# Kernel optimization log

Measured on AMD Instinct MI355X. Metric: run time of the kernel, lower is better.

The kernel has to match this reference:

```python
import jax, jax.numpy as jnp
import numpy as np

N = 50000
IN_C = 128
HID = 64
HEADS = 4
OUT_C = 64
E_RAND = 800000
NEG_SLOPE = 0.2  # PyG GATConv default


def setup_inputs() -> dict:
    key = jax.random.key(0)
    ks = jax.random.split(key, 10)
    x = jax.random.normal(ks[0], (N, IN_C), dtype=jnp.float32)
    src = jax.random.randint(ks[1], (E_RAND,), 0, N)
    dst = jax.random.randint(ks[2], (E_RAND,), 0, N)
    loops = jnp.arange(N)
    # PyG GATConv adds self-loops by default; append them here
    edge_index = jnp.stack([jnp.concatenate([src, loops]),
                            jnp.concatenate([dst, loops])], axis=0).astype(jnp.int64)
    s = 0.05
    W1 = jax.random.normal(ks[3], (IN_C, HEADS * HID), dtype=jnp.float32) * s
    att_src1 = jax.random.normal(ks[4], (HEADS, HID), dtype=jnp.float32) * s
    att_dst1 = jax.random.normal(ks[5], (HEADS, HID), dtype=jnp.float32) * s
    b1 = jnp.zeros((HEADS * HID,), dtype=jnp.float32)
    W2 = jax.random.normal(ks[6], (HEADS * HID, OUT_C), dtype=jnp.float32) * s
    att_src2 = jax.random.normal(ks[7], (1, OUT_C), dtype=jnp.float32) * s
    att_dst2 = jax.random.normal(ks[8], (1, OUT_C), dtype=jnp.float32) * s
    b2 = jnp.zeros((OUT_C,), dtype=jnp.float32)
    return {"x": x, "edge_index": edge_index, "W1": W1, "att_src1": att_src1,
            "att_dst1": att_dst1, "b1": b1, "W2": W2, "att_src2": att_src2,
            "att_dst2": att_dst2, "b2": b2}


def gat_conv(x, src, dst, W, att_src, att_dst, bias, heads, ch, concat):
    n = x.shape[0]
    h = (x @ W).reshape(n, heads, ch)                      # [N,H,C]
    a_src = jnp.einsum('nhc,hc->nh', h, att_src)           # [N,H]
    a_dst = jnp.einsum('nhc,hc->nh', h, att_dst)
    e = jax.nn.leaky_relu(a_src[src] + a_dst[dst], NEG_SLOPE)  # [E,H]
    # segment softmax over incoming edges of each dst node
    m = jax.ops.segment_max(e, dst, num_segments=n)
    ex = jnp.exp(e - m[dst])
    ssum = jax.ops.segment_sum(ex, dst, num_segments=n)
    alpha = ex / jnp.where(ssum[dst] > 0, ssum[dst], 1.0)  # [E,H]
    msg = h[src] * alpha[:, :, None]                        # [E,H,C]
    out = jax.ops.segment_sum(msg, dst, num_segments=n)     # [N,H,C]
    out = out.reshape(n, heads * ch) if concat else out.mean(axis=1)
    return out + bias


def reference(x, edge_index, W1, att_src1, att_dst1, b1, W2, att_src2, att_dst2, b2):
    src, dst = edge_index[0], edge_index[1]
    # eval mode: feature dropout and attention dropout are identity
    h = gat_conv(x, src, dst, W1, att_src1, att_dst1, b1, HEADS, HID, True)
    h = jax.nn.elu(h)
    out = gat_conv(h, src, dst, W2, att_src2, att_dst2, b2, 1, OUT_C, False)
    return out
```

## Files before the change

kernel.cpp:

```cpp
#include <hip/hip_runtime.h>
#include <hip/hip_bf16.h>

#define IN_C 128
#define HID 64
#define HEADS 4
#define OUT_C 64
#define NEG_SLOPE 0.2f

typedef __attribute__((ext_vector_type(8))) short bfrag8;
typedef __attribute__((ext_vector_type(4))) float facc4;

__device__ __forceinline__ float bf16u_to_f(unsigned short u) {
  return __uint_as_float(((unsigned)u) << 16);
}
__device__ __forceinline__ float lof(unsigned u) {
  return __uint_as_float(u << 16);
}
__device__ __forceinline__ float hif(unsigned u) {
  return __uint_as_float(u & 0xffff0000u);
}
__device__ __forceinline__ unsigned short f_to_bf16u(float f) {
  return __bfloat16_as_ushort(__float2bfloat16(f));
}
__device__ __forceinline__ float leaky(float x) {
  return (x > 0.f) ? x : NEG_SLOPE * x;
}

__global__ __launch_bounds__(256) void setup_kernel(
    const float* __restrict__ W1, const float* __restrict__ W2,
    unsigned short* __restrict__ B1img, unsigned short* __restrict__ B2img,
    int* __restrict__ deg, int n) {
  int bid = blockIdx.x;
  if (bid < 24) {
    int i = bid * 256 + threadIdx.x;
    if (i < 4096) {
      int g = i & 7, nn = (i >> 3) & 255, kt = i >> 11;
      unsigned short q[8];
#pragma unroll
      for (int e = 0; e < 8; ++e)
        q[e] = f_to_bf16u(W1[(size_t)(kt * 64 + g * 8 + e) * 256 + nn]);
      *reinterpret_cast<uint4*>(
          &B1img[kt * 16384 + nn * 64 + ((g ^ (nn & 7)) << 3)]) =
          *reinterpret_cast<const uint4*>(q);
    } else if (i < 4096 + 2048) {
      int j = i - 4096;
      int g = j & 7, nn = (j >> 3) & 63, kt = j >> 9;
      unsigned short q[8];
#pragma unroll
      for (int e = 0; e < 8; ++e)
        q[e] = f_to_bf16u(W2[(size_t)(kt * 64 + g * 8 + e) * 64 + nn]);
      *reinterpret_cast<uint4*>(
          &B2img[kt * 4096 + nn * 64 + ((g ^ (nn & 7)) << 3)]) =
          *reinterpret_cast<const uint4*>(q);
    }
  } else {
    int i = (bid - 24) * 1024 + threadIdx.x * 4;
    if (i < n)
      *reinterpret_cast<int4*>(&deg[i]) = make_int4(0, 0, 0, 0);
  }
}

__global__ __launch_bounds__(256) void gemm1_hist_kernel(
    const float* __restrict__ A, const unsigned short* __restrict__ B1img,
    const float* __restrict__ att_src, const float* __restrict__ att_dst,
    unsigned short* __restrict__ Hout, float* __restrict__ a_src,
    float* __restrict__ a_dst, int M, int G1,
    const int* __restrict__ dst, int E, int* __restrict__ deg,
    int* __restrict__ rank) {
  __shared__ unsigned short As[64 * 64];
  __shared__ unsigned short Bs[256 * 64];
  const int t = threadIdx.x;

  if ((int)blockIdx.x >= G1) {
    int e0 = ((int)blockIdx.x - G1) * 1024 + t * 4;
    if (e0 + 3 < E) {
      int4 d4 = *reinterpret_cast<const int4*>(&dst[e0]);
      int4 r4;
      r4.x = atomicAdd(&deg[d4.x], 1);
      r4.y = atomicAdd(&deg[d4.y], 1);
      r4.z = atomicAdd(&deg[d4.z], 1);
      r4.w = atomicAdd(&deg[d4.w], 1);
      *reinterpret_cast<int4*>(&rank[e0]) = r4;
    } else {
      for (int e = e0; e < E; ++e) rank[e] = atomicAdd(&deg[dst[e]], 1);
    }
    return;
  }

  const int wid = t >> 6, lane = t & 63;
  const int lg = lane >> 4, li = lane & 15;
  const int bm = blockIdx.x * 64;

  facc4 acc[16];
#pragma unroll
  for (int fn = 0; fn < 16; ++fn) acc[fn] = (facc4)(0.f);

#pragma unroll
  for (int kt = 0; kt < 2; ++kt) {
#pragma unroll
    for (int p = 0; p < 2; ++p) {
      int flat = t + p * 256;
      int row = flat >> 3, g = flat & 7;
      int gr = bm + row;
      float4 v0 = make_float4(0.f, 0.f, 0.f, 0.f), v1 = v0;
      if (gr < M) {
        const float* src = &A[(size_t)gr * 128 + kt * 64 + g * 8];
        v0 = *reinterpret_cast<const float4*>(src);
        v1 = *reinterpret_cast<const float4*>(src + 4);
      }
      unsigned short q[8];
      q[0] = f_to_bf16u(v0.x); q[1] = f_to_bf16u(v0.y);
      q[2] = f_to_bf16u(v0.z); q[3] = f_to_bf16u(v0.w);
      q[4] = f_to_bf16u(v1.x); q[5] = f_to_bf16u(v1.y);
      q[6] = f_to_bf16u(v1.z); q[7] = f_to_bf16u(v1.w);
      *reinterpret_cast<uint4*>(&As[row * 64 + ((g ^ (row & 7)) << 3)]) =
          *reinterpret_cast<const uint4*>(q);
    }
#pragma unroll
    for (int p = 0; p < 8; ++p) {
      int gi = t + p * 256;
      *reinterpret_cast<uint4*>(&Bs[gi * 8]) =
          *reinterpret_cast<const uint4*>(&B1img[kt * 16384 + gi * 8]);
    }
    __syncthreads();
#pragma unroll
    for (int ks = 0; ks < 2; ++ks) {
      int arow = wid * 16 + li;
      int gk = ks * 4 + lg;
      bfrag8 a = *reinterpret_cast<const bfrag8*>(
          &As[arow * 64 + ((gk ^ (arow & 7)) << 3)]);
#pragma unroll
      for (int fn = 0; fn < 16; ++fn) {
        int col = fn * 16 + li;
        bfrag8 b = *reinterpret_cast<const bfrag8*>(
            &Bs[col * 64 + ((gk ^ (col & 7)) << 3)]);
        acc[fn] =
            __builtin_amdgcn_mfma_f32_16x16x32_bf16(a, b, acc[fn], 0, 0, 0);
      }
    }
    __syncthreads();
  }

#pragma unroll
  for (int reg = 0; reg < 4; ++reg) {
    int row = bm + wid * 16 + lg * 4 + reg;
    if (row < M) {
#pragma unroll
      for (int fn = 0; fn < 16; ++fn)
        Hout[(size_t)row * 256 + fn * 16 + li] = f_to_bf16u(acc[fn][reg]);
    }
#pragma unroll
    for (int h = 0; h < 4; ++h) {
      float ps = 0.f, pd = 0.f;
#pragma unroll
      for (int q = 0; q < 4; ++q) {
        int fn = h * 4 + q;
        float c = acc[fn][reg];
        ps += c * att_src[fn * 16 + li];
        pd += c * att_dst[fn * 16 + li];
      }
#pragma unroll
      for (int m = 1; m < 16; m <<= 1) {
        ps += __shfl_xor(ps, m);
        pd += __shfl_xor(pd, m);
      }
      if (row < M && li == 0) {
        a_src[(size_t)row * 4 + h] = ps;
        a_dst[(size_t)row * 4 + h] = pd;
      }
    }
  }
}

__global__ __launch_bounds__(256) void mfma_gemm2(
    const unsigned short* __restrict__ A, const unsigned short* __restrict__ B2img,
    const float* __restrict__ att_src, const float* __restrict__ att_dst,
    unsigned short* __restrict__ Hout, float* __restrict__ a_src,
    float* __restrict__ a_dst, int M) {
  __shared__ unsigned short As[64 * 64];
  __shared__ unsigned short Bs[64 * 64];
  const int t = threadIdx.x;
  const int wid = t >> 6, lane = t & 63;
  const int lg = lane >> 4, li = lane & 15;
  const int bm = blockIdx.x * 64;

  facc4 acc[4];
#pragma unroll
  for (int fn = 0; fn < 4; ++fn) acc[fn] = (facc4)(0.f);

#pragma unroll
  for (int kt = 0; kt < 4; ++kt) {
#pragma unroll
    for (int p = 0; p < 2; ++p) {
      int flat = t + p * 256;
      int row = flat >> 3, g = flat & 7;
      int gr = bm + row;
      uint4 v = make_uint4(0, 0, 0, 0);
      if (gr < M)
        v = *reinterpret_cast<const uint4*>(&A[(size_t)gr * 256 + kt * 64 + g * 8]);
      *reinterpret_cast<uint4*>(&As[row * 64 + ((g ^ (row & 7)) << 3)]) = v;
    }
#pragma unroll
    for (int p = 0; p < 2; ++p) {
      int gi = t + p * 256;
      *reinterpret_cast<uint4*>(&Bs[gi * 8]) =
          *reinterpret_cast<const uint4*>(&B2img[kt * 4096 + gi * 8]);
    }
    __syncthreads();
#pragma unroll
    for (int ks = 0; ks < 2; ++ks) {
      int arow = wid * 16 + li;
      int gk = ks * 4 + lg;
      bfrag8 a = *reinterpret_cast<const bfrag8*>(
          &As[arow * 64 + ((gk ^ (arow & 7)) << 3)]);
#pragma unroll
      for (int fn = 0; fn < 4; ++fn) {
        int col = fn * 16 + li;
        bfrag8 b = *reinterpret_cast<const bfrag8*>(
            &Bs[col * 64 + ((gk ^ (col & 7)) << 3)]);
        acc[fn] =
            __builtin_amdgcn_mfma_f32_16x16x32_bf16(a, b, acc[fn], 0, 0, 0);
      }
    }
    __syncthreads();
  }

  float s_att[4], d_att[4];
#pragma unroll
  for (int fn = 0; fn < 4; ++fn) {
    s_att[fn] = att_src[fn * 16 + li];
    d_att[fn] = att_dst[fn * 16 + li];
  }
#pragma unroll
  for (int reg = 0; reg < 4; ++reg) {
    int row = bm + wid * 16 + lg * 4 + reg;
    float ps = 0.f, pd = 0.f;
#pragma unroll
    for (int fn = 0; fn < 4; ++fn) {
      float c = acc[fn][reg];
      ps += c * s_att[fn];
      pd += c * d_att[fn];
    }
#pragma unroll
    for (int m = 1; m < 16; m <<= 1) {
      ps += __shfl_xor(ps, m);
      pd += __shfl_xor(pd, m);
    }
    if (row < M) {
#pragma unroll
      for (int fn = 0; fn < 4; ++fn)
        Hout[(size_t)row * 64 + fn * 16 + li] = f_to_bf16u(acc[fn][reg]);
      if (li == 0) {
        a_src[row] = ps;
        a_dst[row] = pd;
      }
    }
  }
}

__device__ __forceinline__ int pad4(int d) { return (d + 3) & ~3; }

__global__ __launch_bounds__(256) void scan_partial_kernel(
    const int* __restrict__ deg, int n, int* __restrict__ partials) {
  __shared__ int sm[256];
  int t = threadIdx.x;
  int i = blockIdx.x * 256 + t;
  sm[t] = (i < n) ? pad4(deg[i]) : 0;
  __syncthreads();
  for (int off = 128; off > 0; off >>= 1) {
    if (t < off) sm[t] += sm[t + off];
    __syncthreads();
  }
  if (t == 0) partials[blockIdx.x] = sm[0];
}

__global__ __launch_bounds__(256) void scan_expand_kernel(
    const int* __restrict__ deg, int n, const int* __restrict__ partials,
    int nb, int* __restrict__ offsets, int* __restrict__ ssrc) {
  __shared__ int smp[256];
  __shared__ int sm[256];
  int t = threadIdx.x;
  smp[t] = (t < nb) ? partials[t] : 0;
  __syncthreads();
  for (int off = 1; off < 256; off <<= 1) {
    int u = (t >= off) ? smp[t - off] : 0;
    __syncthreads();
    smp[t] += u;
    __syncthreads();
  }
  int base = (blockIdx.x > 0) ? smp[blockIdx.x - 1] : 0;
  int i = blockIdx.x * 256 + t;
  int d = (i < n) ? deg[i] : 0;
  int v = pad4(d);
  sm[t] = v;
  __syncthreads();
  for (int off = 1; off < 256; off <<= 1) {
    int u = (t >= off) ? sm[t - off] : 0;
    __syncthreads();
    sm[t] += u;
    __syncthreads();
  }
  int excl = sm[t] - v + base;
  if (i < n) {
    offsets[i] = excl;
    for (int k = d; k < v; ++k) ssrc[excl + k] = -1;
  }
}

__global__ void scatter_kernel(const int* __restrict__ src,
                               const int* __restrict__ dst,
                               const int* __restrict__ rank,
                               const int* __restrict__ offsets, int E,
                               int* __restrict__ ssrc) {
  int e0 = (blockIdx.x * blockDim.x + threadIdx.x) * 4;
  if (e0 + 3 < E) {
    int4 s4 = *reinterpret_cast<const int4*>(&src[e0]);
    int4 d4 = *reinterpret_cast<const int4*>(&dst[e0]);
    int4 r4 = *reinterpret_cast<const int4*>(&rank[e0]);
    ssrc[offsets[d4.x] + r4.x] = s4.x;
    ssrc[offsets[d4.y] + r4.y] = s4.y;
    ssrc[offsets[d4.z] + r4.z] = s4.z;
    ssrc[offsets[d4.w] + r4.w] = s4.w;
  } else {
    for (int e = e0; e < E; ++e) ssrc[offsets[dst[e]] + rank[e]] = src[e];
  }
}

__global__ __launch_bounds__(256) void agg1_kernel(
    const unsigned short* __restrict__ h1, const float* __restrict__ as1,
    const float* __restrict__ ad1, const int* __restrict__ ssrc,
    const int* __restrict__ offsets, const int* __restrict__ deg,
    const float* __restrict__ bias, unsigned short* __restrict__ out,
    int n_nodes) {
  int wave = (int)((blockIdx.x * blockDim.x + threadIdx.x) >> 6);
  int lane = threadIdx.x & 63;
  if (wave >= n_nodes) return;
  int head = lane >> 4;
  int off = offsets[wave];
  int cnt = deg[wave];
  int last = ((cnt + 3) >> 2) - 1;
  const int* S_ = ssrc + off;
  float ad = ad1[wave * 4 + head];
  const int pbase = lane & 48;

  auto ldS = [&](int g) {
    return *reinterpret_cast<const int4*>(S_ + min(g, last) * 4);
  };
  auto gK = [&](int4 S, float* a_out) {
    int sk = (lane & 1) ? S.y : S.x;
    int sk2 = (lane & 1) ? S.w : S.z;
    sk = (lane & 2) ? sk2 : sk;
    *a_out = as1[max(sk, 0) * 4 + head];
    return sk;
  };
  auto mkP = [&](int sk, float a) {
    float pk = (sk >= 0) ? __expf(leaky(a + ad)) : 0.f;
    return make_float4(__shfl(pk, pbase), __shfl(pk, pbase + 1),
                       __shfl(pk, pbase + 2), __shfl(pk, pbase + 3));
  };
  auto gat = [&](int s) {
    return *reinterpret_cast<const uint2*>(
        &h1[(size_t)max(s, 0) * 256 + lane * 4]);
  };

  float l = 0.f, a0 = 0.f, a1 = 0.f, a2 = 0.f, a3 = 0.f;

  int4 Sg0 = ldS(0), Sg1 = ldS(1);
  int4 SgP = ldS(2);
  uint2 HA0 = gat(Sg0.x), HA1 = gat(Sg0.y), HA2 = gat(Sg0.z), HA3 = gat(Sg0.w);
  uint2 HB0 = gat(Sg1.x), HB1 = gat(Sg1.y), HB2 = gat(Sg1.z), HB3 = gat(Sg1.w);
  float aKA, aKB;
  int skA = gK(Sg0, &aKA);
  int skB = gK(Sg1, &aKB);
  float4 PA = mkP(skA, aKA), PB;

  int j = 0;
  auto step = [&](float4& Pc, float4& Pn, uint2& Hc0, uint2& Hc1, uint2& Hc2,
                  uint2& Hc3, int& skN, float& aKN, int skC, float aKC) {
    Pn = mkP(skC, aKC);
    skN = gK(SgP, &aKN);
    l += Pc.x + Pc.y + Pc.z + Pc.w;
    a0 += Pc.x * lof(Hc0.x) + Pc.y * lof(Hc1.x) + Pc.z * lof(Hc2.x) +
          Pc.w * lof(Hc3.x);
    a1 += Pc.x * hif(Hc0.x) + Pc.y * hif(Hc1.x) + Pc.z * hif(Hc2.x) +
          Pc.w * hif(Hc3.x);
    a2 += Pc.x * lof(Hc0.y) + Pc.y * lof(Hc1.y) + Pc.z * lof(Hc2.y) +
          Pc.w * lof(Hc3.y);
    a3 += Pc.x * hif(Hc0.y) + Pc.y * hif(Hc1.y) + Pc.z * hif(Hc2.y) +
          Pc.w * hif(Hc3.y);
    Hc0 = gat(SgP.x); Hc1 = gat(SgP.y); Hc2 = gat(SgP.z); Hc3 = gat(SgP.w);
    SgP = ldS(j + 3);
  };

  for (;;) {
    step(PA, PB, HA0, HA1, HA2, HA3, skA, aKA, skB, aKB);
    if (++j > last) break;
    step(PB, PA, HB0, HB1, HB2, HB3, skB, aKB, skA, aKA);
    if (++j > last) break;
  }

  float inv = 1.0f / l;
  int col = lane * 4;
  float4 b4 = *reinterpret_cast<const float4*>(&bias[col]);
  float o0 = a0 * inv + b4.x;
  float o1 = a1 * inv + b4.y;
  float o2 = a2 * inv + b4.z;
  float o3 = a3 * inv + b4.w;
  o0 = o0 > 0.f ? o0 : __expf(o0) - 1.f;
  o1 = o1 > 0.f ? o1 : __expf(o1) - 1.f;
  o2 = o2 > 0.f ? o2 : __expf(o2) - 1.f;
  o3 = o3 > 0.f ? o3 : __expf(o3) - 1.f;
  unsigned short q[4];
  q[0] = f_to_bf16u(o0); q[1] = f_to_bf16u(o1);
  q[2] = f_to_bf16u(o2); q[3] = f_to_bf16u(o3);
  *reinterpret_cast<ushort4*>(&out[(size_t)wave * 256 + col]) =
      *reinterpret_cast<const ushort4*>(q);
}

__global__ __launch_bounds__(256) void agg2_kernel(
    const unsigned short* __restrict__ h2, const float* __restrict__ as2,
    const float* __restrict__ ad2, const int* __restrict__ ssrc,
    const int* __restrict__ offsets, const int* __restrict__ deg,
    const float* __restrict__ bias, float* __restrict__ out, int n_nodes) {
  int wave = (int)((blockIdx.x * blockDim.x + threadIdx.x) >> 6);
  int lane = threadIdx.x & 63;
  if (wave >= n_nodes) return;
  int off = offsets[wave];
  int cnt = deg[wave];
  int last = ((cnt + 3) >> 2) - 1;
  const int* S_ = ssrc + off;
  float ad = ad2[wave];

  auto ldS = [&](int g) {
    return *reinterpret_cast<const int4*>(S_ + min(g, last) * 4);
  };
  auto gK = [&](int4 S, float* a_out) {
    int sk = (lane & 1) ? S.y : S.x;
    int sk2 = (lane & 1) ? S.w : S.z;
    sk = (lane & 2) ? sk2 : sk;
    *a_out = as2[max(sk, 0)];
    return sk;
  };
  auto mkP = [&](int sk, float a) {
    float pk = (sk >= 0) ? __expf(leaky(a + ad)) : 0.f;
    return make_float4(__shfl(pk, 0), __shfl(pk, 1), __shfl(pk, 2),
                       __shfl(pk, 3));
  };
  auto gat = [&](int s) { return h2[(size_t)max(s, 0) * 64 + lane]; };

  float l = 0.f, acc = 0.f;

  int4 Sg0 = ldS(0), Sg1 = ldS(1);
  int4 SgP = ldS(2);
  unsigned short HA0 = gat(Sg0.x), HA1 = gat(Sg0.y), HA2 = gat(Sg0.z),
                 HA3 = gat(Sg0.w);
  unsigned short HB0 = gat(Sg1.x), HB1 = gat(Sg1.y), HB2 = gat(Sg1.z),
                 HB3 = gat(Sg1.w);
  float aKA, aKB;
  int skA = gK(Sg0, &aKA);
  int skB = gK(Sg1, &aKB);
  float4 PA = mkP(skA, aKA), PB;

  int j = 0;
  auto step = [&](float4& Pc, float4& Pn, unsigned short& Hc0,
                  unsigned short& Hc1, unsigned short& Hc2, unsigned short& Hc3,
                  int& skN, float& aKN, int skC, float aKC) {
    Pn = mkP(skC, aKC);
    skN = gK(SgP, &aKN);
    l += Pc.x + Pc.y + Pc.z + Pc.w;
    acc += Pc.x * bf16u_to_f(Hc0) + Pc.y * bf16u_to_f(Hc1) +
           Pc.z * bf16u_to_f(Hc2) + Pc.w * bf16u_to_f(Hc3);
    Hc0 = gat(SgP.x); Hc1 = gat(SgP.y); Hc2 = gat(SgP.z); Hc3 = gat(SgP.w);
    SgP = ldS(j + 3);
  };

  for (;;) {
    step(PA, PB, HA0, HA1, HA2, HA3, skA, aKA, skB, aKB);
    if (++j > last) break;
    step(PB, PA, HB0, HB1, HB2, HB3, skB, aKB, skA, aKA);
    if (++j > last) break;
  }

  out[(size_t)wave * 64 + lane] = acc / l + bias[lane];
}

extern "C" void kernel_launch(void* const* d_in, const int* in_sizes, int n_in,
                              void* d_out, int out_size, void* d_ws,
                              size_t ws_size, hipStream_t stream) {
  const float* x = (const float*)d_in[0];
  const int* edge_index = (const int*)d_in[1];
  const float* W1 = (const float*)d_in[2];
  const float* att_src1 = (const float*)d_in[3];
  const float* att_dst1 = (const float*)d_in[4];
  const float* b1 = (const float*)d_in[5];
  const float* W2 = (const float*)d_in[6];
  const float* att_src2 = (const float*)d_in[7];
  const float* att_dst2 = (const float*)d_in[8];
  const float* b2 = (const float*)d_in[9];

  const int n = in_sizes[0] / IN_C;
  const int E = in_sizes[1] / 2;
  const int* src = edge_index;
  const int* dst = edge_index + E;
  const int nb = (n + 255) / 256;
  const int stride = (E + 4 * n + 3) & ~3;

  char* ws = (char*)d_ws;
  size_t off = 0;
  auto carve = [&](size_t bytes) -> void* {
    void* p = ws + off;
    off = (off + bytes + 255) & ~(size_t)255;
    return p;
  };
  unsigned short* h1b = (unsigned short*)carve((size_t)n * 256 * 2);
  unsigned short* hact = (unsigned short*)carve((size_t)n * 256 * 2);
  unsigned short* h2b = (unsigned short*)carve((size_t)n * 64 * 2);
  unsigned short* B1img = (unsigned short*)carve(32768 * 2);
  unsigned short* B2img = (unsigned short*)carve(16384 * 2);
  float* as1 = (float*)carve((size_t)n * 4 * 4);
  float* ad1 = (float*)carve((size_t)n * 4 * 4);
  float* as2 = (float*)carve((size_t)n * 4);
  float* ad2 = (float*)carve((size_t)n * 4);
  int* deg = (int*)carve((size_t)n * 4);
  int* offsets = (int*)carve((size_t)n * 4);
  int* rank = (int*)carve((size_t)E * 4);
  int* ssrc = (int*)carve((size_t)stride * 4);
  int* partials = (int*)carve((size_t)nb * 4);

  {
    int zb = (n + 1023) / 1024;
    setup_kernel<<<24 + zb, 256, 0, stream>>>(W1, W2, B1img, B2img, deg, n);
  }
  {
    int G1 = (n + 63) / 64;
    int H = (E + 1023) / 1024;
    gemm1_hist_kernel<<<G1 + H, 256, 0, stream>>>(
        x, B1img, att_src1, att_dst1, h1b, as1, ad1, n, G1, dst, E, deg, rank);
  }
  scan_partial_kernel<<<nb, 256, 0, stream>>>(deg, n, partials);
  scan_expand_kernel<<<nb, 256, 0, stream>>>(deg, n, partials, nb, offsets,
                                             ssrc);
  scatter_kernel<<<(E / 4 + 255) / 256, 256, 0, stream>>>(src, dst, rank,
                                                          offsets, E, ssrc);
  agg1_kernel<<<(n * 64 + 255) / 256, 256, 0, stream>>>(
      h1b, as1, ad1, ssrc, offsets, deg, b1, hact, n);
  mfma_gemm2<<<(n + 63) / 64, 256, 0, stream>>>(hact, B2img, att_src2,
                                                att_dst2, h2b, as2, ad2, n);
  agg2_kernel<<<(n * 64 + 255) / 256, 256, 0, stream>>>(
      h2b, as2, ad2, ssrc, offsets, deg, b2, (float*)d_out, n);
}
```

Measured before the change: 270.2 us.

## Fuse CSR scan and scatter into one cooperative kernel; restructure agg2 lanes

```diff
diff --git a/kernel.cpp b/kernel.cpp
--- a/kernel.cpp
+++ b/kernel.cpp
@@ -1,5 +1,8 @@
 #include <hip/hip_runtime.h>
 #include <hip/hip_bf16.h>
+#include <hip/hip_cooperative_groups.h>
+
+namespace cg = cooperative_groups;
 
 #define IN_C 128
 #define HID 64
@@ -260,69 +263,71 @@
 
 __device__ __forceinline__ int pad4(int d) { return (d + 3) & ~3; }
 
-__global__ __launch_bounds__(256) void scan_partial_kernel(
-    const int* __restrict__ deg, int n, int* __restrict__ partials) {
+__global__ __launch_bounds__(256) void csr_coop_kernel(
+    const int* __restrict__ deg, int n, int nb, int* __restrict__ partials,
+    int* __restrict__ offsets, int* __restrict__ ssrc,
+    const int* __restrict__ src, const int* __restrict__ dst,
+    const int* __restrict__ rank, int E) {
+  cg::grid_group grid = cg::this_grid();
   __shared__ int sm[256];
+  __shared__ int smp[256];
   int t = threadIdx.x;
-  int i = blockIdx.x * 256 + t;
-  sm[t] = (i < n) ? pad4(deg[i]) : 0;
-  __syncthreads();
-  for (int off = 128; off > 0; off >>= 1) {
-    if (t < off) sm[t] += sm[t + off];
-    __syncthreads();
-  }
-  if (t == 0) partials[blockIdx.x] = sm[0];
-}
-
-__global__ __launch_bounds__(256) void scan_expand_kernel(
-    const int* __restrict__ deg, int n, const int* __restrict__ partials,
-    int nb, int* __restrict__ offsets, int* __restrict__ ssrc) {
-  __shared__ int smp[256];
-  __shared__ int sm[256];
-  int t = threadIdx.x;
-  smp[t] = (t < nb) ? partials[t] : 0;
-  __syncthreads();
-  for (int off = 1; off < 256; off <<= 1) {
-    int u = (t >= off) ? smp[t - off] : 0;
-    __syncthreads();
-    smp[t] += u;
-    __syncthreads();
-  }
-  int base = (blockIdx.x > 0) ? smp[blockIdx.x - 1] : 0;
-  int i = blockIdx.x * 256 + t;
-  int d = (i < n) ? deg[i] : 0;
-  int v = pad4(d);
-  sm[t] = v;
-  __syncthreads();
-  for (int off = 1; off < 256; off <<= 1) {
-    int u = (t >= off) ? sm[t - off] : 0;
-    __syncthreads();
-    sm[t] += u;
-    __syncthreads();
-  }
-  int excl = sm[t] - v + base;
-  if (i < n) {
-    offsets[i] = excl;
-    for (int k = d; k < v; ++k) ssrc[excl + k] = -1;
-  }
-}
-
-__global__ void scatter_kernel(const int* __restrict__ src,
-                               const int* __restrict__ dst,
-                               const int* __restrict__ rank,
-                               const int* __restrict__ offsets, int E,
-                               int* __restrict__ ssrc) {
-  int e0 = (blockIdx.x * blockDim.x + threadIdx.x) * 4;
-  if (e0 + 3 < E) {
-    int4 s4 = *reinterpret_cast<const int4*>(&src[e0]);
-    int4 d4 = *reinterpret_cast<const int4*>(&dst[e0]);
-    int4 r4 = *reinterpret_cast<const int4*>(&rank[e0]);
-    ssrc[offsets[d4.x] + r4.x] = s4.x;
-    ssrc[offsets[d4.y] + r4.y] = s4.y;
-    ssrc[offsets[d4.z] + r4.z] = s4.z;
-    ssrc[offsets[d4.w] + r4.w] = s4.w;
-  } else {
-    for (int e = e0; e < E; ++e) ssrc[offsets[dst[e]] + rank[e]] = src[e];
+  int b = blockIdx.x;
+
+  if (b < nb) {
+    int i = b * 256 + t;
+    sm[t] = (i < n) ? pad4(deg[i]) : 0;
+    __syncthreads();
+    for (int off = 128; off > 0; off >>= 1) {
+      if (t < off) sm[t] += sm[t + off];
+      __syncthreads();
+    }
+    if (t == 0) partials[b] = sm[0];
+  }
+  grid.sync();
+
+  if (b < nb) {
+    smp[t] = (t < nb) ? partials[t] : 0;
+    __syncthreads();
+    for (int off = 1; off < 256; off <<= 1) {
+      int u = (t >= off) ? smp[t - off] : 0;
+      __syncthreads();
+      smp[t] += u;
+      __syncthreads();
+    }
+    int base = (b > 0) ? smp[b - 1] : 0;
+    int i = b * 256 + t;
+    int d = (i < n) ? deg[i] : 0;
+    int v = pad4(d);
+    sm[t] = v;
+    __syncthreads();
+    for (int off = 1; off < 256; off <<= 1) {
+      int u = (t >= off) ? sm[t - off] : 0;
+      __syncthreads();
+      sm[t] += u;
+      __syncthreads();
+    }
+    int excl = sm[t] - v + base;
+    if (i < n) {
+      offsets[i] = excl;
+      for (int k = d; k < v; ++k) ssrc[excl + k] = -1;
+    }
+  }
+  grid.sync();
+
+  int stride4 = gridDim.x * 256 * 4;
+  for (int e0 = (b * 256 + t) * 4; e0 < E; e0 += stride4) {
+    if (e0 + 3 < E) {
+      int4 s4 = *reinterpret_cast<const int4*>(&src[e0]);
+      int4 d4 = *reinterpret_cast<const int4*>(&dst[e0]);
+      int4 r4 = *reinterpret_cast<const int4*>(&rank[e0]);
+      ssrc[offsets[d4.x] + r4.x] = s4.x;
+      ssrc[offsets[d4.y] + r4.y] = s4.y;
+      ssrc[offsets[d4.z] + r4.z] = s4.z;
+      ssrc[offsets[d4.w] + r4.w] = s4.w;
+    } else {
+      for (int e = e0; e < E; ++e) ssrc[offsets[dst[e]] + rank[e]] = src[e];
+    }
   }
 }
 
@@ -430,58 +435,59 @@
   int last = ((cnt + 3) >> 2) - 1;
   const int* S_ = ssrc + off;
   float ad = ad2[wave];
-
-  auto ldS = [&](int g) {
-    return *reinterpret_cast<const int4*>(S_ + min(g, last) * 4);
-  };
-  auto gK = [&](int4 S, float* a_out) {
-    int sk = (lane & 1) ? S.y : S.x;
-    int sk2 = (lane & 1) ? S.w : S.z;
-    sk = (lane & 2) ? sk2 : sk;
-    *a_out = as2[max(sk, 0)];
-    return sk;
-  };
-  auto mkP = [&](int sk, float a) {
-    float pk = (sk >= 0) ? __expf(leaky(a + ad)) : 0.f;
-    return make_float4(__shfl(pk, 0), __shfl(pk, 1), __shfl(pk, 2),
-                       __shfl(pk, 3));
-  };
-  auto gat = [&](int s) { return h2[(size_t)max(s, 0) * 64 + lane]; };
-
-  float l = 0.f, acc = 0.f;
-
-  int4 Sg0 = ldS(0), Sg1 = ldS(1);
-  int4 SgP = ldS(2);
-  unsigned short HA0 = gat(Sg0.x), HA1 = gat(Sg0.y), HA2 = gat(Sg0.z),
-                 HA3 = gat(Sg0.w);
-  unsigned short HB0 = gat(Sg1.x), HB1 = gat(Sg1.y), HB2 = gat(Sg1.z),
-                 HB3 = gat(Sg1.w);
-  float aKA, aKB;
-  int skA = gK(Sg0, &aKA);
-  int skB = gK(Sg1, &aKB);
-  float4 PA = mkP(skA, aKA), PB;
+  const int eq = lane >> 4;
+  const int ch4 = (lane & 15) * 4;
+
+  auto ldS = [&](int g) { return S_[min(g, last) * 4 + eq]; };
+  auto gat = [&](int s) {
+    return *reinterpret_cast<const uint2*>(&h2[(size_t)max(s, 0) * 64 + ch4]);
+  };
+
+  float lsum = 0.f, c0 = 0.f, c1 = 0.f, c2 = 0.f, c3 = 0.f;
+
+  int sA = ldS(0);
+  uint2 HA = gat(sA);
+  float aA = as2[max(sA, 0)];
+  int sB = ldS(1);
+  uint2 HB = gat(sB);
+  float aB = as2[max(sB, 0)];
 
   int j = 0;
-  auto step = [&](float4& Pc, float4& Pn, unsigned short& Hc0,
-                  unsigned short& Hc1, unsigned short& Hc2, unsigned short& Hc3,
-                  int& skN, float& aKN, int skC, float aKC) {
-    Pn = mkP(skC, aKC);
-    skN = gK(SgP, &aKN);
-    l += Pc.x + Pc.y + Pc.z + Pc.w;
-    acc += Pc.x * bf16u_to_f(Hc0) + Pc.y * bf16u_to_f(Hc1) +
-           Pc.z * bf16u_to_f(Hc2) + Pc.w * bf16u_to_f(Hc3);
-    Hc0 = gat(SgP.x); Hc1 = gat(SgP.y); Hc2 = gat(SgP.z); Hc3 = gat(SgP.w);
-    SgP = ldS(j + 3);
+  auto step = [&](int& sC, uint2& HC, float& aC) {
+    float e = aC + ad;
+    e = (e > 0.f) ? e : NEG_SLOPE * e;
+    float p = (sC >= 0) ? __expf(e) : 0.f;
+    lsum += p;
+    c0 += p * lof(HC.x);
+    c1 += p * hif(HC.x);
+    c2 += p * lof(HC.y);
+    c3 += p * hif(HC.y);
+    int sN = ldS(j + 2);
+    sC = sN;
+    HC = gat(sN);
+    aC = as2[max(sN, 0)];
   };
 
   for (;;) {
-    step(PA, PB, HA0, HA1, HA2, HA3, skA, aKA, skB, aKB);
+    step(sA, HA, aA);
     if (++j > last) break;
-    step(PB, PA, HB0, HB1, HB2, HB3, skB, aKB, skA, aKA);
+    step(sB, HB, aB);
     if (++j > last) break;
   }
 
-  out[(size_t)wave * 64 + lane] = acc / l + bias[lane];
+  lsum += __shfl_xor(lsum, 16); lsum += __shfl_xor(lsum, 32);
+  c0 += __shfl_xor(c0, 16); c0 += __shfl_xor(c0, 32);
+  c1 += __shfl_xor(c1, 16); c1 += __shfl_xor(c1, 32);
+  c2 += __shfl_xor(c2, 16); c2 += __shfl_xor(c2, 32);
+  c3 += __shfl_xor(c3, 16); c3 += __shfl_xor(c3, 32);
+
+  if (lane < 16) {
+    float inv = 1.0f / lsum;
+    float4 b4 = *reinterpret_cast<const float4*>(&bias[ch4]);
+    float4 o = make_float4(c0 * inv + b4.x, c1 * inv + b4.y, c2 * inv + b4.z,
+                           c3 * inv + b4.w);
+    *reinterpret_cast<float4*>(&out[(size_t)wave * 64 + ch4]) = o;
+  }
 }
 
 extern "C" void kernel_launch(void* const* d_in, const int* in_sizes, int n_in,
@@ -537,11 +543,15 @@
     gemm1_hist_kernel<<<G1 + H, 256, 0, stream>>>(
         x, B1img, att_src1, att_dst1, h1b, as1, ad1, n, G1, dst, E, deg, rank);
   }
-  scan_partial_kernel<<<nb, 256, 0, stream>>>(deg, n, partials);
-  scan_expand_kernel<<<nb, 256, 0, stream>>>(deg, n, partials, nb, offsets,
-                                             ssrc);
-  scatter_kernel<<<(E / 4 + 255) / 256, 256, 0, stream>>>(src, dst, rank,
-                                                          offsets, E, ssrc);
+  {
+    int gb = 832;
+    int n_ = n, nb_ = nb, E_ = E;
+    void* args[] = {(void*)&deg,  (void*)&n_,      (void*)&nb_,
+                    (void*)&partials, (void*)&offsets, (void*)&ssrc,
+                    (void*)&src,  (void*)&dst,     (void*)&rank, (void*)&E_};
+    hipLaunchCooperativeKernel((void*)csr_coop_kernel, dim3(gb), dim3(256),
+                               args, 0, stream);
+  }
   agg1_kernel<<<(n * 64 + 255) / 256, 256, 0, stream>>>(
       h1b, as1, ad1, ssrc, offsets, deg, b1, hact, n);
   mfma_gemm2<<<(n + 63) / 64, 256, 0, stream>>>(hact, B2img, att_src2,
```

Result: slower. 469.3 us (+73.7%).
